# Optimization experiments

Hardware: AMD Instinct MI355X
Metric: run time of the kernel (lower is better)

Reference implementation:

```python
import jax, jax.numpy as jnp
import numpy as np

N = 50000   # nodes
E = 800000  # edges (avg degree 16)
IN, H, OUT = 128, 128, 128


def _lin(key, fan_in, fan_out):
    s = 1.0 / np.sqrt(fan_in)
    return jax.random.uniform(key, (fan_in, fan_out), minval=-s, maxval=s, dtype=jnp.float32)


def setup_inputs() -> dict:
    key = jax.random.key(0)
    ks = jax.random.split(key, 12)
    inp = {
        "x": jax.random.normal(ks[0], (N, IN), dtype=jnp.float32),
        "edge_index": jax.random.randint(ks[1], (2, E), 0, N, dtype=jnp.int64),
        # layer 1: in -> hidden
        "Wl1": _lin(ks[2], IN, H), "b1": jnp.zeros((H,), jnp.float32), "Wr1": _lin(ks[3], IN, H),
        # layer 2: hidden -> hidden
        "Wl2": _lin(ks[4], H, H), "b2": jnp.zeros((H,), jnp.float32), "Wr2": _lin(ks[5], H, H),
        # layer 3: hidden -> out
        "Wl3": _lin(ks[6], H, OUT), "b3": jnp.zeros((OUT,), jnp.float32), "Wr3": _lin(ks[7], H, OUT),
    }
    return inp


def _sage_conv(x, src, dst, inv_deg, Wl, b, Wr):
    # mean-aggregate neighbor messages: gather from src, scatter-sum to dst
    msg = jnp.take(x, src, axis=0)                       # [E, d]
    agg = jax.ops.segment_sum(msg, dst, num_segments=N)  # [N, d]
    mean = agg * inv_deg[:, None]                        # scatter-mean (0 for isolated)
    return mean @ Wl + b + x @ Wr


def reference(x, edge_index, Wl1, b1, Wr1, Wl2, b2, Wr2, Wl3, b3, Wr3):
    src, dst = edge_index[0], edge_index[1]
    deg = jax.ops.segment_sum(jnp.ones((E,), jnp.float32), dst, num_segments=N)
    inv_deg = jnp.where(deg > 0, 1.0 / jnp.maximum(deg, 1.0), 0.0)

    h = _sage_conv(x, src, dst, inv_deg, Wl1, b1, Wr1)
    h = jax.nn.relu(h)  # dropout p=0.5 is identity in eval mode
    h = _sage_conv(h, src, dst, inv_deg, Wl2, b2, Wr2)
    h = jax.nn.relu(h)
    h = _sage_conv(h, src, dst, inv_deg, Wl3, b3, Wr3)
    return h
```

## Files before the change

kernel.cpp:

```cpp
#include <hip/hip_runtime.h>


#define D 128

typedef __attribute__((ext_vector_type(8))) short bf16x8;
typedef __attribute__((ext_vector_type(4))) float f32x4;

__device__ inline ushort f2bf(float f) {
  union { float f; unsigned u; } v; v.f = f;
  unsigned r = v.u + 0x7fffu + ((v.u >> 16) & 1u);
  return (ushort)(r >> 16);
}
__device__ inline float bf2f(ushort h) {
  union { unsigned u; float f; } v; v.u = ((unsigned)h) << 16;
  return v.f;
}

__global__ __launch_bounds__(256) void k_bhist(const int* __restrict__ dst,
                                               int* __restrict__ bhist, int E, int NB) {
  __shared__ int h[512];
  int t = threadIdx.x;
  for (int i = t; i < NB; i += 256) h[i] = 0;
  __syncthreads();
  int beg = blockIdx.x * 4096;
  int end = min(beg + 4096, E);
  for (int i = beg + t; i < end; i += 256) atomicAdd(&h[dst[i] >> 7], 1);
  __syncthreads();
  for (int i = t; i < NB; i += 256)
    if (h[i]) atomicAdd(&bhist[i], h[i]);
}

__global__ __launch_bounds__(512) void k_bscan(const int* __restrict__ bhist,
                                               int* __restrict__ bbase,
                                               int* __restrict__ bcur,
                                               int* __restrict__ offN, int NB) {
  __shared__ int part[512];
  int t = threadIdx.x;
  part[t] = (t < NB) ? bhist[t] : 0;
  __syncthreads();
  for (int d = 1; d < 512; d <<= 1) {
    int x = part[t];
    int a = (t >= d) ? part[t - d] : 0;
    __syncthreads();
    part[t] = x + a;
    __syncthreads();
  }
  if (t < NB) {
    int b = (t == 0) ? 0 : part[t - 1];
    bbase[t] = b;
    bcur[t] = b;
  }
  if (t == NB - 1) *offN = part[t];
}

__global__ __launch_bounds__(256) void k_bucket(const int* __restrict__ src,
                                                const int* __restrict__ dst,
                                                int* __restrict__ bcur,
                                                unsigned* __restrict__ ebuf,
                                                int E, int NB) {
  __shared__ int h[512];
  __shared__ int base[512];
  int t = threadIdx.x;
  for (int i = t; i < NB; i += 256) h[i] = 0;
  __syncthreads();
  int beg = blockIdx.x * 4096;
  int end = min(beg + 4096, E);
  for (int i = beg + t; i < end; i += 256) atomicAdd(&h[dst[i] >> 7], 1);
  __syncthreads();
  for (int i = t; i < NB; i += 256) {
    int c = h[i];
    base[i] = c ? atomicAdd(&bcur[i], c) : 0;
    h[i] = 0;
  }
  __syncthreads();
  for (int i = beg + t; i < end; i += 256) {
    int d = dst[i];
    int b = d >> 7;
    int r = atomicAdd(&h[b], 1);
    ebuf[base[b] + r] = (((unsigned)src[i]) << 16) | (unsigned)d;
  }
}

__global__ __launch_bounds__(256) void k_csr(const unsigned* __restrict__ ebuf,
                                             const int* __restrict__ bbase,
                                             const int* __restrict__ bhist,
                                             int* __restrict__ off,
                                             float* __restrict__ invd,
                                             int* __restrict__ srcs, int N) {
  __shared__ int dcount[128];
  __shared__ int dloc[128];
  int b = blockIdx.x;
  int t = threadIdx.x;
  int beg = bbase[b];
  int end = beg + bhist[b];
  if (t < 128) dcount[t] = 0;
  __syncthreads();
  for (int i = beg + t; i < end; i += 256) atomicAdd(&dcount[ebuf[i] & 127], 1);
  __syncthreads();
  if (t < 128) dloc[t] = dcount[t];
  __syncthreads();
  for (int d = 1; d < 128; d <<= 1) {
    int x = 0, a = 0;
    if (t < 128) {
      x = dloc[t];
      if (t >= d) a = dloc[t - d];
    }
    __syncthreads();
    if (t < 128) dloc[t] = x + a;
    __syncthreads();
  }
  if (t < 128) {
    int node = b * 128 + t;
    if (node < N) {
      int ex = beg + dloc[t] - dcount[t];
      off[node] = ex;
      int c = dcount[t];
      invd[node] = c > 0 ? 1.0f / (float)c : 0.0f;
      dcount[t] = ex;
    }
  }
  __syncthreads();
  for (int i = beg + t; i < end; i += 256) {
    unsigned p = ebuf[i];
    int slot = atomicAdd(&dcount[p & 127], 1);
    srcs[slot] = (int)(p >> 16);
  }
}

__global__ void k_cast(const float* __restrict__ x, ushort* __restrict__ xb, int total4) {
  int i = blockIdx.x * blockDim.x + threadIdx.x;
  if (i >= total4) return;
  float4 v = *reinterpret_cast<const float4*>(x + (size_t)i * 4);
  ushort4 o;
  o.x = f2bf(v.x); o.y = f2bf(v.y); o.z = f2bf(v.z); o.w = f2bf(v.w);
  *reinterpret_cast<ushort4*>(xb + (size_t)i * 4) = o;
}

__global__ void k_pack3(const float* __restrict__ Wl1, const float* __restrict__ Wr1,
                        const float* __restrict__ Wl2, const float* __restrict__ Wr2,
                        const float* __restrict__ Wl3, const float* __restrict__ Wr3,
                        ushort* __restrict__ Bp) {
  int gidx = blockIdx.x * blockDim.x + threadIdx.x;
  int layer = gidx >> 15;
  int idx = gidx & 32767;
  const float* Wl = (layer == 0) ? Wl1 : (layer == 1) ? Wl2 : Wl3;
  const float* Wr = (layer == 0) ? Wr1 : (layer == 1) ? Wr2 : Wr3;
  int kk = idx >> 12;
  int ct = (idx >> 9) & 7;
  int l  = (idx >> 3) & 63;
  int j  = idx & 7;
  int k = kk * 32 + ((l >> 4) << 3) + j;
  int col = ct * 16 + (l & 15);
  float v = (k < 128) ? Wl[k * 128 + col] : Wr[(k - 128) * 128 + col];
  Bp[gidx] = f2bf(v);
}

__global__ void k_gather(const ushort* __restrict__ hin, const int* __restrict__ off,
                         const int* __restrict__ srcs, const float* __restrict__ invd,
                         ushort* __restrict__ meanb, int N) {
  int t = blockIdx.x * blockDim.x + threadIdx.x;
  int n = t >> 4;
  if (n >= N) return;
  int c = (t & 15) * 8;
  int lo = off[n], hi = off[n + 1];
  float acc[8] = {0.f, 0.f, 0.f, 0.f, 0.f, 0.f, 0.f, 0.f};
  for (int e = lo; e < hi; ++e) {
    int s = srcs[e];
    bf16x8 v = *reinterpret_cast<const bf16x8*>(hin + (size_t)s * D + c);
#pragma unroll
    for (int j = 0; j < 8; ++j) acc[j] += bf2f((ushort)v[j]);
  }
  float w = invd[n];
  bf16x8 ov;
#pragma unroll
  for (int j = 0; j < 8; ++j) ov[j] = (short)f2bf(acc[j] * w);
  *reinterpret_cast<bf16x8*>(meanb + (size_t)n * D + c) = ov;
}

template <int RELU, int FINAL>
__global__ __launch_bounds__(256) void k_combine(const ushort* __restrict__ meanb,
                                                 const ushort* __restrict__ hb,
                                                 const ushort* __restrict__ Bpack,
                                                 const float* __restrict__ bias,
                                                 float* __restrict__ outf,
                                                 ushort* __restrict__ outh, int N) {
  int l = threadIdx.x & 63;
  int w = threadIdx.x >> 6;
  int row0 = blockIdx.x * 64 + w * 16;
  int lr = l & 15;
  int kgrp = l >> 4;
  int arow = row0 + lr;
  if (arow >= N) arow = N - 1;
  size_t abase = (size_t)arow * D;

  f32x4 acc[8];
#pragma unroll
  for (int ct = 0; ct < 8; ++ct) {
    float bv = bias[ct * 16 + lr];
    acc[ct] = (f32x4){bv, bv, bv, bv};
  }

#pragma unroll
  for (int kk = 0; kk < 8; ++kk) {
    const ushort* asrc = (kk < 4) ? meanb : hb;
    int klocal = ((kk & 3) << 5) + (kgrp << 3);
    bf16x8 a = *reinterpret_cast<const bf16x8*>(asrc + abase + klocal);
    const ushort* bb = Bpack + ((size_t)kk << 12) + ((size_t)l << 3);
#pragma unroll
    for (int ct = 0; ct < 8; ++ct) {
      bf16x8 b = *reinterpret_cast<const bf16x8*>(bb + (ct << 9));
      acc[ct] = __builtin_amdgcn_mfma_f32_16x16x32_bf16(a, b, acc[ct], 0, 0, 0);
    }
  }

#pragma unroll
  for (int ct = 0; ct < 8; ++ct) {
    int c = ct * 16 + lr;
#pragma unroll
    for (int r = 0; r < 4; ++r) {
      int rr = row0 + kgrp * 4 + r;
      if (rr < N) {
        float v = acc[ct][r];
        if (RELU) v = fmaxf(v, 0.f);
        if (FINAL) outf[(size_t)rr * D + c] = v;
        else outh[(size_t)rr * D + c] = f2bf(v);
      }
    }
  }
}

extern "C" void kernel_launch(void* const* d_in, const int* in_sizes, int n_in,
                              void* d_out, int out_size, void* d_ws, size_t ws_size,
                              hipStream_t stream) {
  const float* x   = (const float*)d_in[0];
  const int*   ei  = (const int*)d_in[1];
  const float* Wl1 = (const float*)d_in[2];
  const float* b1  = (const float*)d_in[3];
  const float* Wr1 = (const float*)d_in[4];
  const float* Wl2 = (const float*)d_in[5];
  const float* b2  = (const float*)d_in[6];
  const float* Wr2 = (const float*)d_in[7];
  const float* Wl3 = (const float*)d_in[8];
  const float* b3  = (const float*)d_in[9];
  const float* Wr3 = (const float*)d_in[10];
  float* out = (float*)d_out;

  int N = in_sizes[0] / D;
  int E = in_sizes[1] / 2;
  const int* srcp = ei;
  const int* dstp = ei + E;
  int NB = (N + 127) >> 7;

  char* p = (char*)d_ws;
  auto carve = [&](size_t bytes) {
    void* r = (void*)p;
    p += (bytes + 255) & ~(size_t)255;
    return r;
  };
  int*      bhist = (int*)carve((size_t)512 * 4);
  int*      bbase = (int*)carve((size_t)512 * 4);
  int*      bcur  = (int*)carve((size_t)512 * 4);
  int*      off   = (int*)carve((size_t)(N + 1) * 4);
  float*    invd  = (float*)carve((size_t)N * 4);
  int*      srcs  = (int*)carve((size_t)E * 4);
  unsigned* ebuf  = (unsigned*)carve((size_t)E * 4);
  ushort*   xb    = (ushort*)carve((size_t)N * D * 2);
  ushort*   h1b   = (ushort*)carve((size_t)N * D * 2);
  ushort*   h2b   = (ushort*)carve((size_t)N * D * 2);
  ushort*   meanb = (ushort*)carve((size_t)N * D * 2);
  ushort*   Bp    = (ushort*)carve((size_t)3 * 32768 * 2);

  hipMemsetAsync(bhist, 0, (size_t)NB * 4, stream);
  int ch_blocks = (E + 4095) / 4096;
  k_bhist<<<ch_blocks, 256, 0, stream>>>(dstp, bhist, E, NB);
  k_bscan<<<1, 512, 0, stream>>>(bhist, bbase, bcur, off + N, NB);
  k_bucket<<<ch_blocks, 256, 0, stream>>>(srcp, dstp, bcur, ebuf, E, NB);
  k_csr<<<NB, 256, 0, stream>>>(ebuf, bbase, bhist, off, invd, srcs, N);

  int total4 = N * D / 4;
  k_cast<<<(total4 + 255) / 256, 256, 0, stream>>>(x, xb, total4);
  k_pack3<<<3 * 32768 / 256, 256, 0, stream>>>(Wl1, Wr1, Wl2, Wr2, Wl3, Wr3, Bp);

  int gather_blocks  = (N * 16 + 255) / 256;
  int combine_blocks = (N + 63) / 64;

  k_gather<<<gather_blocks, 256, 0, stream>>>(xb, off, srcs, invd, meanb, N);
  k_combine<1, 0><<<combine_blocks, 256, 0, stream>>>(meanb, xb, Bp, b1, nullptr, h1b, N);
  k_gather<<<gather_blocks, 256, 0, stream>>>(h1b, off, srcs, invd, meanb, N);
  k_combine<1, 0><<<combine_blocks, 256, 0, stream>>>(meanb, h1b, Bp + 32768, b2, nullptr, h2b, N);
  k_gather<<<gather_blocks, 256, 0, stream>>>(h2b, off, srcs, invd, meanb, N);
  k_combine<0, 1><<<combine_blocks, 256, 0, stream>>>(meanb, h2b, Bp + 2 * 32768, b3, out, nullptr, N);
}
```

Before: 219.8 us.

## Fuse neighbor gather-mean into MFMA combine kernel via swizzled LDS tile

Merges the per-layer gather (mean aggregation) and combine (dual GEMM) kernels into one kernel. Each block aggregates 64 nodes into a 16KB XOR-swizzled shared-memory tile, then feeds it directly to the MFMA loop. This removes the meanb global buffer round trip (write plus reread of N*128 bf16 per layer) and half the launches. The trade-off is less gather parallelism per block, since each thread now processes four nodes serially, and a barrier between the phases.

New measurement: 273.3 us. +24.3%, slower.

```diff
diff --git a/kernel.cpp b/kernel.cpp
--- a/kernel.cpp
+++ b/kernel.cpp
@@ -155,41 +155,52 @@
   Bp[gidx] = f2bf(v);
 }
 
-__global__ void k_gather(const ushort* __restrict__ hin, const int* __restrict__ off,
-                         const int* __restrict__ srcs, const float* __restrict__ invd,
-                         ushort* __restrict__ meanb, int N) {
-  int t = blockIdx.x * blockDim.x + threadIdx.x;
-  int n = t >> 4;
-  if (n >= N) return;
-  int c = (t & 15) * 8;
-  int lo = off[n], hi = off[n + 1];
-  float acc[8] = {0.f, 0.f, 0.f, 0.f, 0.f, 0.f, 0.f, 0.f};
-  for (int e = lo; e < hi; ++e) {
-    int s = srcs[e];
-    bf16x8 v = *reinterpret_cast<const bf16x8*>(hin + (size_t)s * D + c);
-#pragma unroll
-    for (int j = 0; j < 8; ++j) acc[j] += bf2f((ushort)v[j]);
-  }
-  float w = invd[n];
-  bf16x8 ov;
-#pragma unroll
-  for (int j = 0; j < 8; ++j) ov[j] = (short)f2bf(acc[j] * w);
-  *reinterpret_cast<bf16x8*>(meanb + (size_t)n * D + c) = ov;
-}
-
 template <int RELU, int FINAL>
-__global__ __launch_bounds__(256) void k_combine(const ushort* __restrict__ meanb,
-                                                 const ushort* __restrict__ hb,
-                                                 const ushort* __restrict__ Bpack,
-                                                 const float* __restrict__ bias,
-                                                 float* __restrict__ outf,
-                                                 ushort* __restrict__ outh, int N) {
-  int l = threadIdx.x & 63;
-  int w = threadIdx.x >> 6;
-  int row0 = blockIdx.x * 64 + w * 16;
+__global__ __launch_bounds__(256) void k_layer(const ushort* __restrict__ hin,
+                                               const int* __restrict__ off,
+                                               const int* __restrict__ srcs,
+                                               const float* __restrict__ invd,
+                                               const ushort* __restrict__ Bpack,
+                                               const float* __restrict__ bias,
+                                               float* __restrict__ outf,
+                                               ushort* __restrict__ outh, int N) {
+  __shared__ ushort smean[64 * D];
+  int t = threadIdx.x;
+  int node0 = blockIdx.x * 64;
+
+  int sub = t & 15;
+  int c = sub * 8;
+#pragma unroll
+  for (int it = 0; it < 4; ++it) {
+    int nl = it * 16 + (t >> 4);
+    int n = node0 + nl;
+    float acc[8] = {0.f, 0.f, 0.f, 0.f, 0.f, 0.f, 0.f, 0.f};
+    if (n < N) {
+      int lo = off[n], hi = off[n + 1];
+      for (int e = lo; e < hi; ++e) {
+        int s = srcs[e];
+        bf16x8 v = *reinterpret_cast<const bf16x8*>(hin + (size_t)s * D + c);
+#pragma unroll
+        for (int j = 0; j < 8; ++j) acc[j] += bf2f((ushort)v[j]);
+      }
+      float wgt = invd[n];
+#pragma unroll
+      for (int j = 0; j < 8; ++j) acc[j] *= wgt;
+    }
+    bf16x8 ov;
+#pragma unroll
+    for (int j = 0; j < 8; ++j) ov[j] = (short)f2bf(acc[j]);
+    int byte = nl * 256 + ((sub * 16) ^ ((nl & 7) << 4));
+    *reinterpret_cast<bf16x8*>(reinterpret_cast<char*>(smean) + byte) = ov;
+  }
+  __syncthreads();
+
+  int l = t & 63;
+  int w = t >> 6;
   int lr = l & 15;
   int kgrp = l >> 4;
-  int arow = row0 + lr;
+  int nlrow = w * 16 + lr;
+  int arow = node0 + nlrow;
   if (arow >= N) arow = N - 1;
   size_t abase = (size_t)arow * D;
 
@@ -202,9 +213,14 @@
 
 #pragma unroll
   for (int kk = 0; kk < 8; ++kk) {
-    const ushort* asrc = (kk < 4) ? meanb : hb;
     int klocal = ((kk & 3) << 5) + (kgrp << 3);
-    bf16x8 a = *reinterpret_cast<const bf16x8*>(asrc + abase + klocal);
+    bf16x8 a;
+    if (kk < 4) {
+      int byte = nlrow * 256 + ((klocal * 2) ^ ((nlrow & 7) << 4));
+      a = *reinterpret_cast<const bf16x8*>(reinterpret_cast<const char*>(smean) + byte);
+    } else {
+      a = *reinterpret_cast<const bf16x8*>(hin + abase + klocal);
+    }
     const ushort* bb = Bpack + ((size_t)kk << 12) + ((size_t)l << 3);
 #pragma unroll
     for (int ct = 0; ct < 8; ++ct) {
@@ -215,15 +231,15 @@
 
 #pragma unroll
   for (int ct = 0; ct < 8; ++ct) {
-    int c = ct * 16 + lr;
+    int col = ct * 16 + lr;
 #pragma unroll
     for (int r = 0; r < 4; ++r) {
-      int rr = row0 + kgrp * 4 + r;
+      int rr = node0 + w * 16 + kgrp * 4 + r;
       if (rr < N) {
         float v = acc[ct][r];
         if (RELU) v = fmaxf(v, 0.f);
-        if (FINAL) outf[(size_t)rr * D + c] = v;
-        else outh[(size_t)rr * D + c] = f2bf(v);
+        if (FINAL) outf[(size_t)rr * D + col] = v;
+        else outh[(size_t)rr * D + col] = f2bf(v);
       }
     }
   }
@@ -267,7 +283,6 @@
   ushort*   xb    = (ushort*)carve((size_t)N * D * 2);
   ushort*   h1b   = (ushort*)carve((size_t)N * D * 2);
   ushort*   h2b   = (ushort*)carve((size_t)N * D * 2);
-  ushort*   meanb = (ushort*)carve((size_t)N * D * 2);
   ushort*   Bp    = (ushort*)carve((size_t)3 * 32768 * 2);
 
   hipMemsetAsync(bhist, 0, (size_t)NB * 4, stream);
@@ -281,13 +296,9 @@
   k_cast<<<(total4 + 255) / 256, 256, 0, stream>>>(x, xb, total4);
   k_pack3<<<3 * 32768 / 256, 256, 0, stream>>>(Wl1, Wr1, Wl2, Wr2, Wl3, Wr3, Bp);
 
-  int gather_blocks  = (N * 16 + 255) / 256;
-  int combine_blocks = (N + 63) / 64;
-
-  k_gather<<<gather_blocks, 256, 0, stream>>>(xb, off, srcs, invd, meanb, N);
-  k_combine<1, 0><<<combine_blocks, 256, 0, stream>>>(meanb, xb, Bp, b1, nullptr, h1b, N);
-  k_gather<<<gather_blocks, 256, 0, stream>>>(h1b, off, srcs, invd, meanb, N);
-  k_combine<1, 0><<<combine_blocks, 256, 0, stream>>>(meanb, h1b, Bp + 32768, b2, nullptr, h2b, N);
-  k_gather<<<gather_blocks, 256, 0, stream>>>(h2b, off, srcs, invd, meanb, N);
-  k_combine<0, 1><<<combine_blocks, 256, 0, stream>>>(meanb, h2b, Bp + 2 * 32768, b3, out, nullptr, N);
-}
+  int layer_blocks = (N + 63) / 64;
+
+  k_layer<1, 0><<<layer_blocks, 256, 0, stream>>>(xb, off, srcs, invd, Bp, b1, nullptr, h1b, N);
+  k_layer<1, 0><<<layer_blocks, 256, 0, stream>>>(h1b, off, srcs, invd, Bp + 32768, b2, nullptr, h2b, N);
+  k_layer<0, 1><<<layer_blocks, 256, 0, stream>>>(h2b, off, srcs, invd, Bp + 2 * 32768, b3, out, nullptr, N);
+}
```

## Gather neighbors with one wavefront per node and shuffled edge indices

Applied to the files above, without the earlier changes.

The mean-aggregation gather now assigns one 64-lane wavefront per node, with each lane holding two bf16 features, instead of 16 threads per node each holding eight. Source indices are loaded cooperatively, one per lane, then broadcast with shuffles, and the edge loop is unrolled by four so several row loads are in flight at once. This is meant to cut redundant index loads and raise memory-level parallelism in the gather. In exchange each lane issues narrow 4-byte loads, and the shuffle broadcasts add instruction overhead.

Result: faster. 199.0 us (-9.5%).

```diff
diff --git a/kernel.cpp b/kernel.cpp
--- a/kernel.cpp
+++ b/kernel.cpp
@@ -155,26 +155,46 @@
   Bp[gidx] = f2bf(v);
 }
 
-__global__ void k_gather(const ushort* __restrict__ hin, const int* __restrict__ off,
-                         const int* __restrict__ srcs, const float* __restrict__ invd,
-                         ushort* __restrict__ meanb, int N) {
-  int t = blockIdx.x * blockDim.x + threadIdx.x;
-  int n = t >> 4;
-  if (n >= N) return;
-  int c = (t & 15) * 8;
-  int lo = off[n], hi = off[n + 1];
-  float acc[8] = {0.f, 0.f, 0.f, 0.f, 0.f, 0.f, 0.f, 0.f};
-  for (int e = lo; e < hi; ++e) {
-    int s = srcs[e];
-    bf16x8 v = *reinterpret_cast<const bf16x8*>(hin + (size_t)s * D + c);
-#pragma unroll
-    for (int j = 0; j < 8; ++j) acc[j] += bf2f((ushort)v[j]);
-  }
-  float w = invd[n];
-  bf16x8 ov;
-#pragma unroll
-  for (int j = 0; j < 8; ++j) ov[j] = (short)f2bf(acc[j] * w);
-  *reinterpret_cast<bf16x8*>(meanb + (size_t)n * D + c) = ov;
+__global__ __launch_bounds__(256) void k_gather(const ushort* __restrict__ hin,
+                                                const int* __restrict__ off,
+                                                const int* __restrict__ srcs,
+                                                const float* __restrict__ invd,
+                                                ushort* __restrict__ meanb, int N) {
+  int wid = blockIdx.x * 4 + (threadIdx.x >> 6);
+  if (wid >= N) return;
+  int lane = threadIdx.x & 63;
+  int lo = off[wid], hi = off[wid + 1];
+  float a0 = 0.f, a1 = 0.f;
+
+  for (int base = lo; base < hi; base += 64) {
+    int cnt = min(64, hi - base);
+    int myidx = (base + lane < hi) ? srcs[base + lane] : 0;
+    int j = 0;
+    for (; j + 3 < cnt; j += 4) {
+      int s0 = __shfl(myidx, j);
+      int s1 = __shfl(myidx, j + 1);
+      int s2 = __shfl(myidx, j + 2);
+      int s3 = __shfl(myidx, j + 3);
+      ushort2 v0 = *reinterpret_cast<const ushort2*>(hin + (size_t)s0 * D + lane * 2);
+      ushort2 v1 = *reinterpret_cast<const ushort2*>(hin + (size_t)s1 * D + lane * 2);
+      ushort2 v2 = *reinterpret_cast<const ushort2*>(hin + (size_t)s2 * D + lane * 2);
+      ushort2 v3 = *reinterpret_cast<const ushort2*>(hin + (size_t)s3 * D + lane * 2);
+      a0 += bf2f(v0.x); a1 += bf2f(v0.y);
+      a0 += bf2f(v1.x); a1 += bf2f(v1.y);
+      a0 += bf2f(v2.x); a1 += bf2f(v2.y);
+      a0 += bf2f(v3.x); a1 += bf2f(v3.y);
+    }
+    for (; j < cnt; ++j) {
+      int s = __shfl(myidx, j);
+      ushort2 v = *reinterpret_cast<const ushort2*>(hin + (size_t)s * D + lane * 2);
+      a0 += bf2f(v.x); a1 += bf2f(v.y);
+    }
+  }
+  float w = invd[wid];
+  ushort2 o;
+  o.x = f2bf(a0 * w);
+  o.y = f2bf(a1 * w);
+  *reinterpret_cast<ushort2*>(meanb + (size_t)wid * D + lane * 2) = o;
 }
 
 template <int RELU, int FINAL>
@@ -281,7 +301,7 @@
   k_cast<<<(total4 + 255) / 256, 256, 0, stream>>>(x, xb, total4);
   k_pack3<<<3 * 32768 / 256, 256, 0, stream>>>(Wl1, Wr1, Wl2, Wr2, Wl3, Wr3, Bp);
 
-  int gather_blocks  = (N * 16 + 255) / 256;
+  int gather_blocks  = (N + 3) / 4;
   int combine_blocks = (N + 63) / 64;
 
   k_gather<<<gather_blocks, 256, 0, stream>>>(xb, off, srcs, invd, meanb, N);
```

## Assign one wavefront per node in gather, splitting edges across four lane groups

Applied to the files above, without the earlier changes.

The gather kernel now gives each node a full 64-lane wavefront instead of 16 lanes. The four 16-lane groups each take a strided subset of the edges, with two loads in flight per iteration, and the partial sums are combined with cross-lane shuffles. This raises memory-level parallelism on the irregular neighbor reads and shortens per-node serial loops. The cost is four times as many threads, plus shuffle reductions, and lanes sit idle on low-degree nodes.

New measurement: 197.6 us. -10.1%, faster.

```diff
diff --git a/kernel.cpp b/kernel.cpp
--- a/kernel.cpp
+++ b/kernel.cpp
@@ -155,26 +155,49 @@
   Bp[gidx] = f2bf(v);
 }
 
-__global__ void k_gather(const ushort* __restrict__ hin, const int* __restrict__ off,
-                         const int* __restrict__ srcs, const float* __restrict__ invd,
-                         ushort* __restrict__ meanb, int N) {
-  int t = blockIdx.x * blockDim.x + threadIdx.x;
-  int n = t >> 4;
-  if (n >= N) return;
-  int c = (t & 15) * 8;
-  int lo = off[n], hi = off[n + 1];
+__global__ __launch_bounds__(256) void k_gather(const ushort* __restrict__ hin,
+                                                const int* __restrict__ off,
+                                                const int* __restrict__ srcs,
+                                                const float* __restrict__ invd,
+                                                ushort* __restrict__ meanb, int N) {
+  int wid = blockIdx.x * 4 + (threadIdx.x >> 6);
+  if (wid >= N) return;
+  int lane = threadIdx.x & 63;
+  int g = lane >> 4;
+  int s = lane & 15;
+  int lo = off[wid], hi = off[wid + 1];
+
   float acc[8] = {0.f, 0.f, 0.f, 0.f, 0.f, 0.f, 0.f, 0.f};
-  for (int e = lo; e < hi; ++e) {
-    int s = srcs[e];
-    bf16x8 v = *reinterpret_cast<const bf16x8*>(hin + (size_t)s * D + c);
-#pragma unroll
-    for (int j = 0; j < 8; ++j) acc[j] += bf2f((ushort)v[j]);
-  }
-  float w = invd[n];
-  bf16x8 ov;
-#pragma unroll
-  for (int j = 0; j < 8; ++j) ov[j] = (short)f2bf(acc[j] * w);
-  *reinterpret_cast<bf16x8*>(meanb + (size_t)n * D + c) = ov;
+  int e = lo + g;
+  for (; e + 4 < hi; e += 8) {
+    int i0 = srcs[e];
+    int i1 = srcs[e + 4];
+    bf16x8 v0 = *reinterpret_cast<const bf16x8*>(hin + (size_t)i0 * D + s * 8);
+    bf16x8 v1 = *reinterpret_cast<const bf16x8*>(hin + (size_t)i1 * D + s * 8);
+#pragma unroll
+    for (int j = 0; j < 8; ++j) acc[j] += bf2f((ushort)v0[j]);
+#pragma unroll
+    for (int j = 0; j < 8; ++j) acc[j] += bf2f((ushort)v1[j]);
+  }
+  if (e < hi) {
+    int i0 = srcs[e];
+    bf16x8 v0 = *reinterpret_cast<const bf16x8*>(hin + (size_t)i0 * D + s * 8);
+#pragma unroll
+    for (int j = 0; j < 8; ++j) acc[j] += bf2f((ushort)v0[j]);
+  }
+
+#pragma unroll
+  for (int j = 0; j < 8; ++j) acc[j] += __shfl_xor(acc[j], 16);
+#pragma unroll
+  for (int j = 0; j < 8; ++j) acc[j] += __shfl_xor(acc[j], 32);
+
+  if (lane < 16) {
+    float w = invd[wid];
+    bf16x8 o;
+#pragma unroll
+    for (int j = 0; j < 8; ++j) o[j] = (short)f2bf(acc[j] * w);
+    *reinterpret_cast<bf16x8*>(meanb + (size_t)wid * D + s * 8) = o;
+  }
 }
 
 template <int RELU, int FINAL>
@@ -281,7 +304,7 @@
   k_cast<<<(total4 + 255) / 256, 256, 0, stream>>>(x, xb, total4);
   k_pack3<<<3 * 32768 / 256, 256, 0, stream>>>(Wl1, Wr1, Wl2, Wr2, Wl3, Wr3, Bp);
 
-  int gather_blocks  = (N * 16 + 255) / 256;
+  int gather_blocks  = (N + 3) / 4;
   int combine_blocks = (N + 63) / 64;
 
   k_gather<<<gather_blocks, 256, 0, stream>>>(xb, off, srcs, invd, meanb, N);
```
